# Optimization experiments

Measured on AMD Instinct MI355X. Metric: run time of the kernel, lower is better.

Reference implementation:

```python
import jax, jax.numpy as jnp
import numpy as np

UNITS = 4096
IN_FEATURES = 4096
TOT_SIZE = UNITS * IN_FEATURES
FINAL_SIZE = TOT_SIZE // 4  # divisible by 4, no padding needed
CLIP_VAL = 100.0


def unpack_ternary(pw, dtype):
    # Matches unpack_ternary_iterative2: for each byte, extract 2-bit fields
    # (lsb first), subtract 1 (codes 0,1,2,3 -> -1,0,1,2), and CONCATENATE
    # the four planes: [field0 of all bytes, field1 of all bytes, ...].
    parts = [(( (pw >> jnp.uint8(2 * i)) & jnp.uint8(3)).astype(dtype) - dtype(1))
             for i in range(4)]
    return jnp.concatenate(parts, axis=-1)


def setup_inputs() -> dict:
    key = jax.random.key(0)
    k_x, k_pw = jax.random.split(key)
    x = jax.random.normal(k_x, (8192, IN_FEATURES), dtype=jnp.float32)
    # packed ternary weights: random uint8 per the module's initializer
    pw = jax.random.randint(k_pw, (FINAL_SIZE,), 0, 256, dtype=jnp.int32).astype(jnp.uint8)
    scale = jnp.ones((UNITS,), dtype=jnp.float32)   # initializer='ones'
    bias = jnp.zeros((UNITS,), dtype=jnp.float32)   # initializer='zeros'
    return {"x": x, "pw": pw, "scale": scale, "bias": bias}


def reference(x, pw, scale, bias):
    dt = x.dtype.type
    unpacked = unpack_ternary(pw, dt)                 # [4 * FINAL_SIZE]
    w = unpacked[:TOT_SIZE].reshape(UNITS, IN_FEATURES)  # [units, in]
    y = jnp.einsum('ti,ui->tu', x, w)                 # matmul with transpose_b
    y = y * scale + bias
    y = jnp.clip(y, -dt(CLIP_VAL), dt(CLIP_VAL))
    return y
```

## Files before the change

### kernel.cpp

```cpp
#include <hip/hip_runtime.h>
#include <stdint.h>

#define MDIM 8192
#define NDIM 4096
#define KDIM 4096
#define FINAL_SZ (NDIM * KDIM / 4)
#define BM 256
#define BN 256
#define BK 64
#define NT (KDIM / BK)

#define CVT_BLOCKS ((MDIM * KDIM / 8) / 256)
#define UNPACK_BLOCKS ((FINAL_SZ / 8) / 256)

typedef __attribute__((ext_vector_type(8))) short short8;
typedef __attribute__((ext_vector_type(4))) float floatx4;

typedef const __attribute__((address_space(1))) void global_cv;
typedef __attribute__((address_space(3))) void lds_v;

__device__ __forceinline__ unsigned short f2bf_rne(float f) {
    union { float f; uint32_t u; } a; a.f = f;
    uint32_t u = a.u;
    u += 0x7FFFu + ((u >> 16) & 1u);
    return (unsigned short)(u >> 16);
}

__device__ __forceinline__ short code2bf(unsigned int c) {
    return (short)((0x40003F800000BF80ull >> (c * 16)) & 0xFFFFull);
}

__global__ void prep_kernel(const float* __restrict__ x, const void* __restrict__ pwv,
                            unsigned short* __restrict__ xb, unsigned short* __restrict__ wb) {
    const int b = blockIdx.x;
    if (b < CVT_BLOCKS) {
        int i = b * 256 + threadIdx.x;
        const float4* xin = (const float4*)x;
        float4 v0 = xin[2 * i];
        float4 v1 = xin[2 * i + 1];
        short8 o;
        o[0] = (short)f2bf_rne(v0.x); o[1] = (short)f2bf_rne(v0.y);
        o[2] = (short)f2bf_rne(v0.z); o[3] = (short)f2bf_rne(v0.w);
        o[4] = (short)f2bf_rne(v1.x); o[5] = (short)f2bf_rne(v1.y);
        o[6] = (short)f2bf_rne(v1.z); o[7] = (short)f2bf_rne(v1.w);
        *(short8*)(xb + (size_t)i * 8) = o;
    } else {
        unsigned int probe = ((const unsigned int*)pwv)[threadIdx.x & 63];
        bool packed = (__ballot(probe > 255u) != 0ull);

        int t = (b - CVT_BLOCKS) * 256 + threadIdx.x;
        unsigned int lo, hi;
        if (packed) {
            uint2 u = ((const uint2*)pwv)[t];
            lo = u.x; hi = u.y;
        } else {
            int4 q0 = ((const int4*)pwv)[2 * t];
            int4 q1 = ((const int4*)pwv)[2 * t + 1];
            lo = (unsigned)(q0.x & 255) | ((unsigned)(q0.y & 255) << 8)
               | ((unsigned)(q0.z & 255) << 16) | ((unsigned)(q0.w & 255) << 24);
            hi = (unsigned)(q1.x & 255) | ((unsigned)(q1.y & 255) << 8)
               | ((unsigned)(q1.z & 255) << 16) | ((unsigned)(q1.w & 255) << 24);
        }
        int j  = t << 3;
        int r  = j >> 12;
        int ci = j & 4095;
#pragma unroll
        for (int p = 0; p < 4; ++p) {
            short8 o;
            o[0] = code2bf((lo >> (2 * p)) & 3u);
            o[1] = code2bf((lo >> (8 + 2 * p)) & 3u);
            o[2] = code2bf((lo >> (16 + 2 * p)) & 3u);
            o[3] = code2bf((lo >> (24 + 2 * p)) & 3u);
            o[4] = code2bf((hi >> (2 * p)) & 3u);
            o[5] = code2bf((hi >> (8 + 2 * p)) & 3u);
            o[6] = code2bf((hi >> (16 + 2 * p)) & 3u);
            o[7] = code2bf((hi >> (24 + 2 * p)) & 3u);
            *(short8*)(wb + (((size_t)((p << 10) + r)) << 12) + ci) = o;
        }
    }
}

#define VWAIT4 asm volatile("s_waitcnt vmcnt(4)" ::: "memory")
#define VWAIT2 asm volatile("s_waitcnt vmcnt(2)" ::: "memory")
#define VWAIT0 asm volatile("s_waitcnt vmcnt(0)" ::: "memory")
#define BARX() do { asm volatile("" ::: "memory"); __builtin_amdgcn_s_barrier(); asm volatile("" ::: "memory"); } while (0)

__global__ __launch_bounds__(512, 2) void gemm_ternary(
    const unsigned short* __restrict__ A,
    const unsigned short* __restrict__ B,
    const float* __restrict__ scale,
    const float* __restrict__ bias,
    float* __restrict__ C) {
    __shared__ __align__(16) unsigned short lA[2][BM * BK];
    __shared__ __align__(16) unsigned short lB[2][BN * BK];

    const int tid  = threadIdx.x;
    const int lane = tid & 63;
    const int wave = tid >> 6;
    const int wm   = wave >> 2;
    const int wn   = wave & 3;
    const int l15  = lane & 15;
    const int lq   = lane >> 4;
    const int lx   = lane & 7;

    const int bid = blockIdx.x;
    const int wg  = ((bid & 7) << 6) | (bid >> 3);
    const int m0  = (wg >> 4) * BM;
    const int n0  = (wg & 15) * BN;

    const int lr = lane >> 3;
    const int cg = (lane & 7) ^ lr;
    const char* gA[4];
    const char* gB[4];
    int offA[4], offB[4];
#pragma unroll
    for (int g = 0; g < 4; ++g) {
        const int ab = ((g & 1) << 7) + ((g >> 1) << 6) + wave * 8;
        offA[g] = ab * BK;
        gA[g] = (const char*)(A + (size_t)(m0 + ab + lr) * KDIM + cg * 8);
        const int bb = ((g & 1) << 7) + ((g >> 1) << 5)
                     + ((wave >> 2) << 6) + ((wave & 3) << 3);
        offB[g] = bb * BK;
        gB[g] = (const char*)(B + (size_t)(n0 + bb + lr) * KDIM + cg * 8);
    }

    int cOff[2];
#pragma unroll
    for (int ks = 0; ks < 2; ++ks)
        cOff[ks] = ((((ks << 2) + lq) ^ lx) << 3);

    floatx4 acc[8][4];
#pragma unroll
    for (int i = 0; i < 8; ++i)
#pragma unroll
        for (int j = 0; j < 4; ++j)
            acc[i][j] = (floatx4)(0.f);

#define SGA(g, sb) do {                                                          \
        __builtin_amdgcn_global_load_lds((global_cv*)gA[g],                      \
            (lds_v*)(&lA[sb][0] + offA[g]), 16, 0, 0);                           \
        gA[g] += BK * 2; } while (0)
#define SGB(g, sb) do {                                                          \
        __builtin_amdgcn_global_load_lds((global_cv*)gB[g],                      \
            (lds_v*)(&lB[sb][0] + offB[g]), 16, 0, 0);                           \
        gB[g] += BK * 2; } while (0)

#define MFMA_Q(AF, BF, MI0, NJ0)                                                 \
    __builtin_amdgcn_s_setprio(1);                                               \
    _Pragma("unroll") for (int i = 0; i < 4; ++i)                                \
    _Pragma("unroll") for (int j = 0; j < 2; ++j)                                \
    _Pragma("unroll") for (int ks = 0; ks < 2; ++ks)                             \
        acc[(MI0) + i][(NJ0) + j] = __builtin_amdgcn_mfma_f32_16x16x32_bf16(     \
            AF[i][ks], BF[j][ks], acc[(MI0) + i][(NJ0) + j], 0, 0, 0);           \
    __builtin_amdgcn_s_setprio(0)

#define TILE_ITER(bufv, DOSTAGE, W0STMT, W1STMT, W3STMT)                         \
  {                                                                              \
    const unsigned short* LA = &lA[bufv][0];                                     \
    const unsigned short* LB = &lB[bufv][0];                                     \
    const int sb = (bufv) ^ 1; (void)sb;                                         \
    short8 a0[4][2], a1[4][2], b0[2][2], b1[2][2];                               \
                   \
    _Pragma("unroll") for (int i = 0; i < 4; ++i)                                \
    _Pragma("unroll") for (int ks = 0; ks < 2; ++ks)                             \
        a0[i][ks] = *(const short8*)(LA + (wm * 128 + i * 16 + l15) * BK + cOff[ks]); \
    _Pragma("unroll") for (int j = 0; j < 2; ++j)                                \
    _Pragma("unroll") for (int ks = 0; ks < 2; ++ks)                             \
        b0[j][ks] = *(const short8*)(LB + (wn * 64 + j * 16 + l15) * BK + cOff[ks]);  \
    if (DOSTAGE) { SGA(0, sb); SGA(1, sb); }                                     \
    BARX();                                                                      \
    MFMA_Q(a0, b0, 0, 0);                                                        \
    W0STMT;                                                                      \
    BARX();                                                                      \
             \
    _Pragma("unroll") for (int j = 0; j < 2; ++j)                                \
    _Pragma("unroll") for (int ks = 0; ks < 2; ++ks)                             \
        b1[j][ks] = *(const short8*)(LB + (wn * 64 + 32 + j * 16 + l15) * BK + cOff[ks]); \
    if (DOSTAGE) { SGB(0, sb); SGB(1, sb); }                                     \
    BARX();                                                                      \
    MFMA_Q(a0, b1, 0, 2);                                                        \
    W1STMT;                                                                      \
    BARX();                                                                      \
             \
    _Pragma("unroll") for (int i = 0; i < 4; ++i)                                \
    _Pragma("unroll") for (int ks = 0; ks < 2; ++ks)                             \
        a1[i][ks] = *(const short8*)(LA + (wm * 128 + 64 + i * 16 + l15) * BK + cOff[ks]); \
    if (DOSTAGE) { SGB(2, sb); SGB(3, sb); }                                     \
    BARX();                                                                      \
    MFMA_Q(a1, b1, 4, 2);                                                        \
    BARX();                                                                      \
                 \
    if (DOSTAGE) { SGA(2, sb); SGA(3, sb); }                                     \
    BARX();                                                                      \
    MFMA_Q(a1, b0, 4, 0);                                                        \
    W3STMT;                                                                      \
    BARX();                                                                      \
  }

    SGA(0, 0); SGA(1, 0); SGB(0, 0); SGB(1, 0);
    SGB(2, 0); SGB(3, 0); SGA(2, 0); SGA(3, 0);
    VWAIT4;
    BARX();

    for (int t = 0; t < NT - 1; ++t) {
        TILE_ITER(t & 1, 1, VWAIT4, VWAIT4, VWAIT4)
    }
    TILE_ITER(1, 0, VWAIT2, VWAIT0, (void)0)

#undef TILE_ITER
#undef MFMA_Q
#undef SGA
#undef SGB

    float sc[4], bi[4];
#pragma unroll
    for (int nj = 0; nj < 4; ++nj) {
        int n  = n0 + wn * 64 + nj * 16 + l15;
        sc[nj] = scale[n];
        bi[nj] = bias[n];
    }
#pragma unroll
    for (int mi = 0; mi < 8; ++mi) {
#pragma unroll
        for (int r = 0; r < 4; ++r) {
            int m = m0 + wm * 128 + mi * 16 + lq * 4 + r;
            float* Crow = C + (size_t)m * NDIM + n0 + wn * 64 + l15;
#pragma unroll
            for (int nj = 0; nj < 4; ++nj) {
                float v = acc[mi][nj][r] * sc[nj] + bi[nj];
                v = fminf(100.f, fmaxf(-100.f, v));
                Crow[nj * 16] = v;
            }
        }
    }
}

extern "C" void kernel_launch(void* const* d_in, const int* in_sizes, int n_in,
                              void* d_out, int out_size, void* d_ws, size_t ws_size,
                              hipStream_t stream) {
    const float* x  = (const float*)d_in[0];
    const void*  pw = d_in[1];
    const float* scale = (const float*)d_in[2];
    const float* bias  = (const float*)d_in[3];
    float* out = (float*)d_out;

    unsigned short* xb = (unsigned short*)d_ws;
    unsigned short* wb = xb + (size_t)MDIM * KDIM;

    prep_kernel<<<CVT_BLOCKS + UNPACK_BLOCKS, 256, 0, stream>>>(x, pw, xb, wb);

    gemm_ternary<<<dim3((MDIM / BM) * (NDIM / BN)), 512, 0, stream>>>(xb, wb, scale, bias, out);
}
```

Baseline: 484.8 us.

## Stage next tile's loads into current LDS buffer as soon as its chunks are consumed

Reorders the global-to-LDS staging so that parts of the tile after next are issued into the current buffer's regions right after their last read. This deepens the prefetch distance, keeping more loads in flight (vmcnt 6 instead of 4). The per-phase waits are dropped and only one wait per half-iteration remains. The cost is more complex buffer hazard reasoning and a correctness risk if a region is overwritten before all waves have read it.

New measurement: 494.7 us. +2.0%, slower.

```diff
diff --git a/kernel.cpp b/kernel.cpp
--- a/kernel.cpp
+++ b/kernel.cpp
@@ -80,8 +80,7 @@
     }
 }
 
-#define VWAIT4 asm volatile("s_waitcnt vmcnt(4)" ::: "memory")
-#define VWAIT2 asm volatile("s_waitcnt vmcnt(2)" ::: "memory")
+#define VWAIT6 asm volatile("s_waitcnt vmcnt(6)" ::: "memory")
 #define VWAIT0 asm volatile("s_waitcnt vmcnt(0)" ::: "memory")
 #define BARX() do { asm volatile("" ::: "memory"); __builtin_amdgcn_s_barrier(); asm volatile("" ::: "memory"); } while (0)
 
@@ -145,6 +144,12 @@
             (lds_v*)(&lB[sb][0] + offB[g]), 16, 0, 0);                           \
         gB[g] += BK * 2; } while (0)
 
+#define SAL(sb) do { SGA(0, sb); SGA(1, sb); } while (0)
+#define SAH(sb) do { SGA(2, sb); SGA(3, sb); } while (0)
+#define SBL(sb) do { SGB(0, sb); SGB(1, sb); } while (0)
+#define SBH(sb) do { SGB(2, sb); SGB(3, sb); } while (0)
+#define NOST    do { } while (0)
+
 #define MFMA_Q(AF, BF, MI0, NJ0)                                                 \
     __builtin_amdgcn_s_setprio(1);                                               \
     _Pragma("unroll") for (int i = 0; i < 4; ++i)                                \
@@ -154,61 +159,65 @@
             AF[i][ks], BF[j][ks], acc[(MI0) + i][(NJ0) + j], 0, 0, 0);           \
     __builtin_amdgcn_s_setprio(0)
 
-#define TILE_ITER(bufv, DOSTAGE, W0STMT, W1STMT, W3STMT)                         \
+#define HALF_ITER(bufv, ST1, ST2, ST3, ST4, W4)                                  \
   {                                                                              \
     const unsigned short* LA = &lA[bufv][0];                                     \
     const unsigned short* LB = &lB[bufv][0];                                     \
-    const int sb = (bufv) ^ 1; (void)sb;                                         \
     short8 a0[4][2], a1[4][2], b0[2][2], b1[2][2];                               \
-                   \
+                                             \
     _Pragma("unroll") for (int i = 0; i < 4; ++i)                                \
     _Pragma("unroll") for (int ks = 0; ks < 2; ++ks)                             \
         a0[i][ks] = *(const short8*)(LA + (wm * 128 + i * 16 + l15) * BK + cOff[ks]); \
     _Pragma("unroll") for (int j = 0; j < 2; ++j)                                \
     _Pragma("unroll") for (int ks = 0; ks < 2; ++ks)                             \
         b0[j][ks] = *(const short8*)(LB + (wn * 64 + j * 16 + l15) * BK + cOff[ks]);  \
-    if (DOSTAGE) { SGA(0, sb); SGA(1, sb); }                                     \
+    ST1;                                                                         \
     BARX();                                                                      \
     MFMA_Q(a0, b0, 0, 0);                                                        \
-    W0STMT;                                                                      \
-    BARX();                                                                      \
-             \
+    BARX();                                                                      \
+                                                \
     _Pragma("unroll") for (int j = 0; j < 2; ++j)                                \
     _Pragma("unroll") for (int ks = 0; ks < 2; ++ks)                             \
         b1[j][ks] = *(const short8*)(LB + (wn * 64 + 32 + j * 16 + l15) * BK + cOff[ks]); \
-    if (DOSTAGE) { SGB(0, sb); SGB(1, sb); }                                     \
+    ST2;                                                                         \
     BARX();                                                                      \
     MFMA_Q(a0, b1, 0, 2);                                                        \
-    W1STMT;                                                                      \
-    BARX();                                                                      \
-             \
+    BARX();                                                                      \
+                                                \
     _Pragma("unroll") for (int i = 0; i < 4; ++i)                                \
     _Pragma("unroll") for (int ks = 0; ks < 2; ++ks)                             \
         a1[i][ks] = *(const short8*)(LA + (wm * 128 + 64 + i * 16 + l15) * BK + cOff[ks]); \
-    if (DOSTAGE) { SGB(2, sb); SGB(3, sb); }                                     \
+    ST3;                                                                         \
     BARX();                                                                      \
     MFMA_Q(a1, b1, 4, 2);                                                        \
     BARX();                                                                      \
-                 \
-    if (DOSTAGE) { SGA(2, sb); SGA(3, sb); }                                     \
+               \
+    ST4;                                                                         \
     BARX();                                                                      \
     MFMA_Q(a1, b0, 4, 0);                                                        \
-    W3STMT;                                                                      \
+    W4;                                                                          \
     BARX();                                                                      \
   }
 
-    SGA(0, 0); SGA(1, 0); SGB(0, 0); SGB(1, 0);
-    SGB(2, 0); SGB(3, 0); SGA(2, 0); SGA(3, 0);
-    VWAIT4;
+    SAL(0); SBL(0); SBH(0); SAH(0);
+    SAL(1); SBL(1); SBH(1);
+    VWAIT6;
     BARX();
 
-    for (int t = 0; t < NT - 1; ++t) {
-        TILE_ITER(t & 1, 1, VWAIT4, VWAIT4, VWAIT4)
-    }
-    TILE_ITER(1, 0, VWAIT2, VWAIT0, (void)0)
-
-#undef TILE_ITER
+    for (int i = 0; i < 31; ++i) {
+        HALF_ITER(0, SAH(1), SAL(0), SBL(0), SBH(0), VWAIT6)
+        HALF_ITER(1, SAH(0), SAL(1), SBL(1), SBH(1), VWAIT6)
+    }
+    HALF_ITER(0, SAH(1), NOST, NOST, NOST, VWAIT0)
+    HALF_ITER(1, NOST, NOST, NOST, NOST, NOST)
+
+#undef HALF_ITER
 #undef MFMA_Q
+#undef SAL
+#undef SAH
+#undef SBL
+#undef SBH
+#undef NOST
 #undef SGA
 #undef SGB
 
```
